# Optimization experiments

Measured on AMD Instinct MI355X. Metric: run time of the kernel, lower is better.

The kernel has to match this reference:

```python
import jax, jax.numpy as jnp
import numpy as np
from jax import lax

V, E, C_OUT, K, NTAGS = 32000, 256, 256, 3, 32
B, T = 64, 2048


def setup_inputs() -> dict:
    key = jax.random.key(0)
    ks = jax.random.split(key, 12)
    inputs = jax.random.randint(ks[0], (B, T), 0, V)
    emb_table = jax.random.normal(ks[1], (V, E), jnp.float32) * 0.02
    emb_table = emb_table.at[1].set(0.0)  # padding_idx=1
    conv1_w = jax.random.normal(ks[2], (C_OUT, E, K), jnp.float32) * 0.02
    conv1_b = jax.random.normal(ks[3], (C_OUT,), jnp.float32) * 0.02
    conv2_w = jax.random.normal(ks[4], (C_OUT, C_OUT, K), jnp.float32) * 0.02
    conv2_b = jax.random.normal(ks[5], (C_OUT,), jnp.float32) * 0.02
    fc_w = jax.random.normal(ks[6], (NTAGS, E), jnp.float32) * 0.02
    fc_b = jax.random.normal(ks[7], (NTAGS,), jnp.float32) * 0.02
    trans = jax.random.normal(ks[8], (NTAGS, NTAGS), jnp.float32) * 0.1
    start_t = jax.random.normal(ks[9], (NTAGS,), jnp.float32) * 0.1
    end_t = jax.random.normal(ks[10], (NTAGS,), jnp.float32) * 0.1
    return {"inputs": inputs, "emb_table": emb_table,
            "conv1_w": conv1_w, "conv1_b": conv1_b,
            "conv2_w": conv2_w, "conv2_b": conv2_b,
            "fc_w": fc_w, "fc_b": fc_b,
            "trans": trans, "start_t": start_t, "end_t": end_t}


def _conv1d(x, w, b):
    # x: [B, C_in, T], w: [C_out, C_in, K], padding=1
    y = lax.conv_general_dilated(x, w, window_strides=(1,), padding=[(1, 1)],
                                 dimension_numbers=("NCH", "OIH", "NCH"))
    return y + b[None, :, None]


def _crf_log_partition(emissions, trans, start_t, end_t):
    # emissions: [B, T, NTAGS] -> logZ per sequence [B]
    em_t = jnp.swapaxes(emissions, 0, 1)  # [T, B, NTAGS]
    alpha0 = start_t[None, :] + em_t[0]   # [B, NTAGS]

    def step(alpha, emit):
        # alpha: [B, C]; broadcast prev-tag x next-tag: [B, C, C]
        scores = alpha[:, :, None] + trans[None, :, :] + emit[:, None, :]
        new_alpha = jax.scipy.special.logsumexp(scores, axis=1)
        return new_alpha, None

    alpha, _ = lax.scan(step, alpha0, em_t[1:])
    return jax.scipy.special.logsumexp(alpha + end_t[None, :], axis=-1)


def reference(inputs, emb_table, conv1_w, conv1_b, conv2_w, conv2_b,
              fc_w, fc_b, trans, start_t, end_t):
    emb = emb_table[inputs]                    # [B, T, E]
    x = jnp.swapaxes(emb, 1, 2)                # [B, E, T]
    x = _conv1d(x, conv1_w, conv1_b)           # [B, C, T]
    x = _conv1d(x, conv2_w, conv2_b)           # [B, C, T]
    h = jnp.swapaxes(x, 1, 2)                  # [B, T, E]  (dropout = identity in eval)
    logits = jnp.einsum("bte,ce->btc", h, fc_w) + fc_b  # [B, T, NTAGS]
    return _crf_log_partition(logits, trans, start_t, end_t)  # [B]
```

## Files before the change

### kernel.cpp

```cpp
#include <hip/hip_runtime.h>
#include <hip/hip_bf16.h>

typedef float f32x4 __attribute__((ext_vector_type(4)));
typedef __bf16 bf16x8 __attribute__((ext_vector_type(8)));
typedef __bf16 bf16x4 __attribute__((ext_vector_type(4)));

__global__ __launch_bounds__(256) void transpose_w(const float* __restrict__ w1,
                                                   const float* __restrict__ w2,
                                                   float* __restrict__ w1t,
                                                   float* __restrict__ w2t) {
  int tid = blockIdx.x * 256 + threadIdx.x;
  if (tid < 196608) {
    float v = w1[tid];
    int k1 = tid % 3;
    int r = tid / 3;
    int e = r & 255;
    int cp = r >> 8;
    w1t[(k1 * 256 + e) * 256 + cp] = v;
  } else {
    int t2 = tid - 196608;
    float v = w2[t2];
    int k2 = t2 % 3;
    int r = t2 / 3;
    int cp = r & 255;
    int c = r >> 8;
    w2t[(k2 * 256 + cp) * 256 + c] = v;
  }
}

__global__ __launch_bounds__(256) void prep_g(const float* __restrict__ fcw,
                                              const float* __restrict__ w2t,
                                              float* __restrict__ G) {
  int tid = blockIdx.x * 256 + threadIdx.x;
  int cp = tid & 255;
  int rest = tid >> 8;
  int n = rest & 31;
  int k2 = rest >> 5;
  const float* wr = w2t + (k2 * 256 + cp) * 256;
  const float* fr = fcw + n * 256;
  float acc = 0.f;
  #pragma unroll 8
  for (int c = 0; c < 256; c += 4) {
    f32x4 a = *(const f32x4*)(fr + c);
    f32x4 bb = *(const f32x4*)(wr + c);
    acc = fmaf(a[0], bb[0], acc); acc = fmaf(a[1], bb[1], acc);
    acc = fmaf(a[2], bb[2], acc); acc = fmaf(a[3], bb[3], acc);
  }
  G[(k2 * 32 + n) * 256 + cp] = acc;
}

__global__ __launch_bounds__(256) void prep_wf(const float* __restrict__ G,
                                               const float* __restrict__ w1t,
                                               const float* __restrict__ b1,
                                               const float* __restrict__ b2,
                                               const float* __restrict__ fcw,
                                               const float* __restrict__ fcb,
                                               __bf16* __restrict__ wfb,
                                               float* __restrict__ C0,
                                               float* __restrict__ CT,
                                               float* __restrict__ bias_tot,
                                               float* __restrict__ c0v,
                                               float* __restrict__ cTv) {
  int tid = blockIdx.x * 256 + threadIdx.x;
  if (tid < 40960) {
    int n = tid & 31;
    int r = tid >> 5;
    int kk = r % 5;
    int e = r / 5;
    float acc = 0.f;
    #pragma unroll
    for (int k2 = 0; k2 < 3; ++k2) {
      int k1 = kk - k2;
      if (k1 < 0 || k1 > 2) continue;
      const float* g = G + (k2 * 32 + n) * 256;
      const float* wr = w1t + (k1 * 256 + e) * 256;
      #pragma unroll 8
      for (int cp = 0; cp < 256; cp += 4) {
        f32x4 a = *(const f32x4*)(g + cp);
        f32x4 bb = *(const f32x4*)(wr + cp);
        acc = fmaf(a[0], bb[0], acc); acc = fmaf(a[1], bb[1], acc);
        acc = fmaf(a[2], bb[2], acc); acc = fmaf(a[3], bb[3], acc);
      }
    }
    int j = kk * 32 + n;
    int jt = j >> 4, jl = j & 15;
    int et = e >> 5, el = e & 31;
    int lane = jl | ((el >> 3) << 4);
    int rr = el & 7;
    wfb[((jt * 8 + et) * 64 + lane) * 8 + rr] = (__bf16)acc;
  } else if (tid < 57344) {
    int t2 = tid - 40960;
    int which = (t2 >= 8192);
    if (which) t2 -= 8192;
    int n = t2 & 31;
    int e = t2 >> 5;
    const float* g = G + ((which ? 2 : 0) * 32 + n) * 256;
    int k1 = which ? 0 : 2;
    const float* wr = w1t + (k1 * 256 + e) * 256;
    float acc = 0.f;
    #pragma unroll 8
    for (int cp = 0; cp < 256; cp += 4) {
      f32x4 a = *(const f32x4*)(g + cp);
      f32x4 bb = *(const f32x4*)(wr + cp);
      acc = fmaf(a[0], bb[0], acc); acc = fmaf(a[1], bb[1], acc);
      acc = fmaf(a[2], bb[2], acc); acc = fmaf(a[3], bb[3], acc);
    }
    (which ? CT : C0)[n * 256 + e] = acc;
  } else if (tid < 57376) {
    int n = tid - 57344;
    float bt = fcb[n];
    for (int c = 0; c < 256; ++c) bt = fmaf(fcw[n * 256 + c], b2[c], bt);
    float s0 = 0.f, s1 = 0.f, s2 = 0.f;
    const float* g0 = G + (0 * 32 + n) * 256;
    const float* g1 = G + (1 * 32 + n) * 256;
    const float* g2 = G + (2 * 32 + n) * 256;
    for (int cp = 0; cp < 256; ++cp) {
      s0 = fmaf(g0[cp], b1[cp], s0);
      s1 = fmaf(g1[cp], b1[cp], s1);
      s2 = fmaf(g2[cp], b1[cp], s2);
    }
    bias_tot[n] = bt + s0 + s1 + s2;
    c0v[n] = s0;
    cTv[n] = s2;
  }
}

__global__ __launch_bounds__(256) void ptab_corr(const float* __restrict__ emb,
                                                 const __bf16* __restrict__ wfb,
                                                 __bf16* __restrict__ P,
                                                 const int* __restrict__ idx,
                                                 const float* __restrict__ C0,
                                                 const float* __restrict__ CT,
                                                 const float* __restrict__ c0v,
                                                 const float* __restrict__ cTv,
                                                 float* __restrict__ corr) {
  __shared__ float red[256];
  if (blockIdx.x < 500) {
    int lane = threadIdx.x & 63;
    int mt = blockIdx.x * 4 + (threadIdx.x >> 6);
    int ln = lane & 15;
    int q = lane >> 4;
    int m = mt * 16 + ln;
    f32x4 acc[10];
    #pragma unroll
    for (int jt = 0; jt < 10; ++jt) acc[jt] = (f32x4){0.f, 0.f, 0.f, 0.f};
    const float* arow = emb + m * 256 + q * 8;
    #pragma unroll
    for (int et = 0; et < 8; ++et) {
      f32x4 a0 = *(const f32x4*)(arow + et * 32);
      f32x4 a1 = *(const f32x4*)(arow + et * 32 + 4);
      bf16x8 af;
      af[0] = (__bf16)a0[0]; af[1] = (__bf16)a0[1];
      af[2] = (__bf16)a0[2]; af[3] = (__bf16)a0[3];
      af[4] = (__bf16)a1[0]; af[5] = (__bf16)a1[1];
      af[6] = (__bf16)a1[2]; af[7] = (__bf16)a1[3];
      #pragma unroll
      for (int jt = 0; jt < 10; ++jt) {
        bf16x8 bfr = *(const bf16x8*)(wfb + ((jt * 8 + et) * 64 + lane) * 8);
        acc[jt] = __builtin_amdgcn_mfma_f32_16x16x32_bf16(af, bfr, acc[jt], 0, 0, 0);
      }
    }
    #pragma unroll
    for (int jt = 0; jt < 10; ++jt) {
      __bf16* pp = P + (mt * 16 + q * 4) * 160 + jt * 16 + ln;
      pp[0]   = (__bf16)acc[jt][0];
      pp[160] = (__bf16)acc[jt][1];
      pp[320] = (__bf16)acc[jt][2];
      pp[480] = (__bf16)acc[jt][3];
    }
  } else {
    int bid = blockIdx.x - 500;
    int b = bid >> 1;
    int which = bid & 1;
    int n = threadIdx.x & 31;
    int part = threadIdx.x >> 5;
    int v = idx[b * 2048 + (which ? 2047 : 0)];
    const float* C = which ? CT : C0;
    const float* er = emb + v * 256 + part * 32;
    const float* cr = C + n * 256 + part * 32;
    float s = 0.f;
    #pragma unroll
    for (int e = 0; e < 32; ++e) s = fmaf(cr[e], er[e], s);
    red[threadIdx.x] = s;
    __syncthreads();
    if (part == 0) {
      float tot = (which ? cTv : c0v)[n];
      #pragma unroll
      for (int p = 0; p < 8; ++p) tot += red[p * 32 + n];
      corr[(which * 64 + b) * 32 + n] = tot;
    }
  }
}

#define LROW 164
__global__ __launch_bounds__(256) void logits_k(const int* __restrict__ idx,
                                                const __bf16* __restrict__ P,
                                                const float* __restrict__ bias_tot,
                                                const float* __restrict__ corr,
                                                __bf16* __restrict__ L) {
  __shared__ __bf16 sp[132 * LROW];
  int b = blockIdx.x >> 4;
  int tb = blockIdx.x & 15;
  int t0 = tb * 128;
  const int* ib = idx + b * 2048;
  for (int ch = threadIdx.x; ch < 2640; ch += 256) {
    int r = ch / 20;
    int part = ch - r * 20;
    int t = t0 - 2 + r;
    uint4 val = {0u, 0u, 0u, 0u};
    if (t >= 0 && t < 2048) {
      int v = ib[t];
      val = *(const uint4*)((const char*)(P + v * 160) + part * 16);
    }
    *(uint4*)((char*)(sp + r * LROW) + part * 16) = val;
  }
  __syncthreads();
  int q = threadIdx.x & 7;
  int ts = threadIdx.x >> 3;
  f32x4 bias = *(const f32x4*)(bias_tot + q * 4);
  f32x4 corr0 = *(const f32x4*)(corr + b * 32 + q * 4);
  f32x4 corrT = *(const f32x4*)(corr + (64 + b) * 32 + q * 4);
  #pragma unroll
  for (int i = 0; i < 4; ++i) {
    int tl = ts + 32 * i;
    int t = t0 + tl;
    f32x4 acc = bias;
    #pragma unroll
    for (int k = 0; k < 5; ++k) {
      bf16x4 pv = *(const bf16x4*)(sp + (tl + k) * LROW + k * 32 + q * 4);
      acc[0] += (float)pv[0]; acc[1] += (float)pv[1];
      acc[2] += (float)pv[2]; acc[3] += (float)pv[3];
    }
    if (t == 0)    acc -= corr0;
    if (t == 2047) acc -= corrT;
    bf16x4 r;
    r[0] = (__bf16)(__expf(acc[0]) * 0.03125f);
    r[1] = (__bf16)(__expf(acc[1]) * 0.03125f);
    r[2] = (__bf16)(__expf(acc[2]) * 0.03125f);
    r[3] = (__bf16)(__expf(acc[3]) * 0.03125f);
    *(bf16x4*)(L + (b * 2048 + t) * 32 + q * 4) = r;
  }
}

__global__ __launch_bounds__(256) void crf_stage1(const __bf16* __restrict__ Lexp,
                                                  const float* __restrict__ trans,
                                                  __bf16* __restrict__ PcB) {
  __shared__ __bf16 sl[4][32 * 40];
  int lane = threadIdx.x & 63;
  int w = threadIdx.x >> 6;
  int chain = blockIdx.x * 4 + w;
  int c = chain >> 6;
  int b = chain & 63;
  int ln = lane & 15;
  int q = lane >> 4;
  float tA0[8], tA1[8];
  #pragma unroll
  for (int e = 0; e < 8; ++e) {
    tA0[e] = __expf(trans[(q * 8 + e) * 32 + ln]);
    tA1[e] = __expf(trans[(q * 8 + e) * 32 + 16 + ln]);
  }
  bf16x8 bf0, bf1;
  #pragma unroll
  for (int e = 0; e < 8; ++e) {
    int k = q * 8 + e;
    bf0[e] = (k == ln) ? (__bf16)1.0f : (__bf16)0.0f;
    bf1[e] = (k == 16 + ln) ? (__bf16)1.0f : (__bf16)0.0f;
  }
  int tstart = c * 32 + 1;
  int total = (c == 63) ? 31 : 32;
  const __bf16* Le = Lexp + (b * 2048 + tstart) * 32;
  __bf16* myS = &sl[w][0];

  auto step = [&](float sc0, float sc1) {
    bf16x8 a0, a1;
    #pragma unroll
    for (int e = 0; e < 8; ++e) {
      a0[e] = (__bf16)(sc0 * tA0[e]);
      a1[e] = (__bf16)(sc1 * tA1[e]);
    }
    f32x4 z = {0.f, 0.f, 0.f, 0.f};
    f32x4 c00 = __builtin_amdgcn_mfma_f32_16x16x32_bf16(a0, bf0, z, 0, 0, 0);
    f32x4 c01 = __builtin_amdgcn_mfma_f32_16x16x32_bf16(a0, bf1, z, 0, 0, 0);
    f32x4 c10 = __builtin_amdgcn_mfma_f32_16x16x32_bf16(a1, bf0, z, 0, 0, 0);
    f32x4 c11 = __builtin_amdgcn_mfma_f32_16x16x32_bf16(a1, bf1, z, 0, 0, 0);
    bf16x4 w00, w01, w10, w11;
    #pragma unroll
    for (int r = 0; r < 4; ++r) {
      w00[r] = (__bf16)c00[r]; w01[r] = (__bf16)c01[r];
      w10[r] = (__bf16)c10[r]; w11[r] = (__bf16)c11[r];
    }
    *(bf16x4*)(myS + (ln) * 40      + q * 4)      = w00;
    *(bf16x4*)(myS + (16 + ln) * 40 + q * 4)      = w01;
    *(bf16x4*)(myS + (ln) * 40      + 16 + q * 4) = w10;
    *(bf16x4*)(myS + (16 + ln) * 40 + 16 + q * 4) = w11;
    bf0 = *(const bf16x8*)(myS + (ln) * 40 + q * 8);
    bf1 = *(const bf16x8*)(myS + (16 + ln) * 40 + q * 8);
  };

  float s0[8], s1[8];
  #pragma unroll
  for (int i = 0; i < 8; ++i) {
    s0[i] = (float)Le[i * 32 + ln];
    s1[i] = (float)Le[i * 32 + 16 + ln];
  }
  int nbatch = total >> 3;
  int rem = total & 7;
  for (int bt = 0; bt < nbatch; ++bt) {
    float n0[8], n1[8];
    bool more = (bt + 1 < nbatch) || (rem != 0 && bt + 1 == nbatch);
    if (more) {
      int bs = (bt + 1) * 8;
      #pragma unroll
      for (int i = 0; i < 8; ++i) {
        int k = bs + i; if (k >= total) k = total - 1;
        n0[i] = (float)Le[k * 32 + ln];
        n1[i] = (float)Le[k * 32 + 16 + ln];
      }
    }
    #pragma unroll
    for (int s = 0; s < 8; ++s) step(s0[s], s1[s]);
    #pragma unroll
    for (int i = 0; i < 8; ++i) { s0[i] = n0[i]; s1[i] = n1[i]; }
  }
  if (rem) {
    #pragma unroll
    for (int s = 0; s < 7; ++s) step(s0[s], s1[s]);
  }
  bf16x8 o0, o1;
  #pragma unroll
  for (int e = 0; e < 8; ++e) {
    o0[e] = myS[(q * 8 + e) * 40 + ln];
    o1[e] = myS[(q * 8 + e) * 40 + 16 + ln];
  }
  __bf16* dst = PcB + ((b * 64 + c) * 64 + lane) * 16;
  *(bf16x8*)(dst)     = o0;
  *(bf16x8*)(dst + 8) = o1;
}

__global__ __launch_bounds__(512) void crf_tail(const __bf16* __restrict__ Lexp,
                                                const __bf16* __restrict__ PcB,
                                                const float* __restrict__ start_t,
                                                const float* __restrict__ end_t,
                                                float* __restrict__ out) {
  __shared__ float sg[8][1024];
  __shared__ __bf16 sl[8][32 * 40];
  int b = blockIdx.x;
  int tid = threadIdx.x;
  int lane = tid & 63;
  int g = tid >> 6;
  int ln = lane & 15;
  int q = lane >> 4;
  const __bf16* base = PcB + ((b * 64 + g * 8) * 64) * 16;
  bf16x8 a0 = *(const bf16x8*)(base + lane * 16);
  bf16x8 a1 = *(const bf16x8*)(base + lane * 16 + 8);
  bf16x8 bf0, bf1;
  #pragma unroll
  for (int e = 0; e < 8; ++e) {
    int k = q * 8 + e;
    bf0[e] = (k == ln) ? (__bf16)1.0f : (__bf16)0.0f;
    bf1[e] = (k == 16 + ln) ? (__bf16)1.0f : (__bf16)0.0f;
  }
  __bf16* myS = &sl[g][0];
  f32x4 c00, c01, c10, c11;
  for (int j = 0; j < 8; ++j) {
    bf16x8 na0, na1;
    if (j < 7) {
      const __bf16* nb = base + (j + 1) * 1024 + lane * 16;
      na0 = *(const bf16x8*)(nb);
      na1 = *(const bf16x8*)(nb + 8);
    }
    f32x4 z = {0.f, 0.f, 0.f, 0.f};
    c00 = __builtin_amdgcn_mfma_f32_16x16x32_bf16(a0, bf0, z, 0, 0, 0);
    c01 = __builtin_amdgcn_mfma_f32_16x16x32_bf16(a0, bf1, z, 0, 0, 0);
    c10 = __builtin_amdgcn_mfma_f32_16x16x32_bf16(a1, bf0, z, 0, 0, 0);
    c11 = __builtin_amdgcn_mfma_f32_16x16x32_bf16(a1, bf1, z, 0, 0, 0);
    if (j < 7) {
      bf16x4 w00, w01, w10, w11;
      #pragma unroll
      for (int r = 0; r < 4; ++r) {
        w00[r] = (__bf16)c00[r]; w01[r] = (__bf16)c01[r];
        w10[r] = (__bf16)c10[r]; w11[r] = (__bf16)c11[r];
      }
      *(bf16x4*)(myS + (ln) * 40      + q * 4)      = w00;
      *(bf16x4*)(myS + (16 + ln) * 40 + q * 4)      = w01;
      *(bf16x4*)(myS + (ln) * 40      + 16 + q * 4) = w10;
      *(bf16x4*)(myS + (16 + ln) * 40 + 16 + q * 4) = w11;
      bf0 = *(const bf16x8*)(myS + (ln) * 40 + q * 8);
      bf1 = *(const bf16x8*)(myS + (16 + ln) * 40 + q * 8);
      a0 = na0; a1 = na1;
    }
  }
  #pragma unroll
  for (int r = 0; r < 4; ++r) {
    sg[g][(ln) * 32      + q * 4 + r]      = c00[r];
    sg[g][(16 + ln) * 32 + q * 4 + r]      = c01[r];
    sg[g][(ln) * 32      + 16 + q * 4 + r] = c10[r];
    sg[g][(16 + ln) * 32 + 16 + q * 4 + r] = c11[r];
  }
  int j2 = tid & 31;
  float u = __expf(start_t[j2]) * (float)Lexp[b * 2048 * 32 + j2] * 32.f;
  __syncthreads();
  float logacc = 0.f;
  #pragma unroll
  for (int gg = 0; gg < 8; ++gg) {
    const float* M = &sg[gg][0];
    float nu0 = 0.f, nu1 = 0.f, nu2 = 0.f, nu3 = 0.f;
    #pragma unroll
    for (int k = 0; k < 32; k += 4) {
      nu0 = fmaf(__shfl(u, k,     32), M[(k)     * 32 + j2], nu0);
      nu1 = fmaf(__shfl(u, k + 1, 32), M[(k + 1) * 32 + j2], nu1);
      nu2 = fmaf(__shfl(u, k + 2, 32), M[(k + 2) * 32 + j2], nu2);
      nu3 = fmaf(__shfl(u, k + 3, 32), M[(k + 3) * 32 + j2], nu3);
    }
    float nu = (nu0 + nu1) + (nu2 + nu3);
    float ssum = nu;
    #pragma unroll
    for (int o = 1; o < 32; o <<= 1) ssum += __shfl_xor(ssum, o, 32);
    u = nu * __builtin_amdgcn_rcpf(ssum);
    logacc += __logf(ssum);
  }
  float term = u * __expf(end_t[j2]);
  #pragma unroll
  for (int o = 1; o < 32; o <<= 1) term += __shfl_xor(term, o, 32);
  if (tid == 0)
    out[b] = logacc + logf(term) + (float)(2047.0 * 5.0 * 0.69314718055994530942);
}

extern "C" void kernel_launch(void* const* d_in, const int* in_sizes, int n_in,
                              void* d_out, int out_size, void* d_ws, size_t ws_size,
                              hipStream_t stream) {
  const int*   idx  = (const int*)d_in[0];
  const float* emb  = (const float*)d_in[1];
  const float* w1   = (const float*)d_in[2];
  const float* b1   = (const float*)d_in[3];
  const float* w2   = (const float*)d_in[4];
  const float* b2   = (const float*)d_in[5];
  const float* fcw  = (const float*)d_in[6];
  const float* fcb  = (const float*)d_in[7];
  const float* trn  = (const float*)d_in[8];
  const float* st   = (const float*)d_in[9];
  const float* en   = (const float*)d_in[10];

  char* ws = (char*)d_ws;
  __bf16* P     = (__bf16*)(ws + 0);
  __bf16* L     = (__bf16*)(ws + 10240000);
  __bf16* PcB   = (__bf16*)(ws + 18628608);
  float*  w1t   = (float*)(ws + 27017216);
  float*  w2t   = (float*)(ws + 27803648);
  __bf16* WfB   = (__bf16*)(ws + 43794432);
  float*  G     = (float*)(ws + 43876352);
  float*  C0    = (float*)(ws + 43974656);
  float*  CT    = (float*)(ws + 44007424);
  float*  bias  = (float*)(ws + 44040192);
  float*  c0v   = (float*)(ws + 44040320);
  float*  cTv   = (float*)(ws + 44040448);
  float*  corr  = (float*)(ws + 44040576);

  transpose_w<<<1536, 256, 0, stream>>>(w1, w2, w1t, w2t);
  prep_g     <<<96,   256, 0, stream>>>(fcw, w2t, G);
  prep_wf    <<<225,  256, 0, stream>>>(G, w1t, b1, b2, fcw, fcb, WfB, C0, CT, bias, c0v, cTv);
  ptab_corr  <<<628,  256, 0, stream>>>(emb, WfB, P, idx, C0, CT, c0v, cTv, corr);
  logits_k   <<<1024, 256, 0, stream>>>(idx, P, bias, corr, L);
  crf_stage1 <<<1024, 256, 0, stream>>>(L, trn, PcB);
  crf_tail   <<<64,   512, 0, stream>>>(L, PcB, st, en, (float*)d_out);
}
```

Measured before the change: 199.7 us.

## Fuse logits computation into CRF stage-1 chunk kernel via shared memory

```diff
diff --git a/kernel.cpp b/kernel.cpp
--- a/kernel.cpp
+++ b/kernel.cpp
@@ -192,86 +192,81 @@
   }
 }
 
-#define LROW 164
-__global__ __launch_bounds__(256) void logits_k(const int* __restrict__ idx,
-                                                const __bf16* __restrict__ P,
-                                                const float* __restrict__ bias_tot,
-                                                const float* __restrict__ corr,
-                                                __bf16* __restrict__ L) {
-  __shared__ __bf16 sp[132 * LROW];
+__global__ __launch_bounds__(256) void logits_crf1(const int* __restrict__ idx,
+                                                   const __bf16* __restrict__ P,
+                                                   const float* __restrict__ bias_tot,
+                                                   const float* __restrict__ corr,
+                                                   const float* __restrict__ trans,
+                                                   __bf16* __restrict__ PcB,
+                                                   float* __restrict__ Lt0) {
+  __shared__ __bf16 sLe[129 * 32];
+  __shared__ __bf16 sl[4][32 * 40];
   int b = blockIdx.x >> 4;
   int tb = blockIdx.x & 15;
   int t0 = tb * 128;
-  const int* ib = idx + b * 2048;
-  for (int ch = threadIdx.x; ch < 2640; ch += 256) {
-    int r = ch / 20;
-    int part = ch - r * 20;
-    int t = t0 - 2 + r;
-    uint4 val = {0u, 0u, 0u, 0u};
-    if (t >= 0 && t < 2048) {
-      int v = ib[t];
-      val = *(const uint4*)((const char*)(P + v * 160) + part * 16);
-    }
-    *(uint4*)((char*)(sp + r * LROW) + part * 16) = val;
+  int tid = threadIdx.x;
+  int lane = tid & 63;
+  int w = tid >> 6;
+  int ln = lane & 15;
+  int q4 = lane >> 4;
+  float tA0[8], tA1[8];
+  #pragma unroll
+  for (int e = 0; e < 8; ++e) {
+    tA0[e] = __expf(trans[(q4 * 8 + e) * 32 + ln]);
+    tA1[e] = __expf(trans[(q4 * 8 + e) * 32 + 16 + ln]);
+  }
+  {
+    int q = tid & 7;
+    int ts0 = tid >> 3;
+    const int* ib = idx + b * 2048;
+    f32x4 bias = *(const f32x4*)(bias_tot + q * 4);
+    f32x4 corr0 = *(const f32x4*)(corr + b * 32 + q * 4);
+    f32x4 corrT = *(const f32x4*)(corr + (64 + b) * 32 + q * 4);
+    int nts = (ts0 == 0 && tb < 15) ? 5 : 4;
+    for (int i = 0; i < nts; ++i) {
+      int ts = ts0 + 32 * i;
+      int t = t0 + ts;
+      f32x4 acc = bias;
+      #pragma unroll
+      for (int k = 0; k < 5; ++k) {
+        int tt = t + k - 2;
+        if (tt >= 0 && tt < 2048) {
+          int v = ib[tt];
+          bf16x4 pv = *(const bf16x4*)(P + v * 160 + k * 32 + q * 4);
+          acc[0] += (float)pv[0]; acc[1] += (float)pv[1];
+          acc[2] += (float)pv[2]; acc[3] += (float)pv[3];
+        }
+      }
+      if (t == 0)    acc -= corr0;
+      if (t == 2047) acc -= corrT;
+      float e0 = __expf(acc[0]) * 0.03125f;
+      float e1 = __expf(acc[1]) * 0.03125f;
+      float e2 = __expf(acc[2]) * 0.03125f;
+      float e3 = __expf(acc[3]) * 0.03125f;
+      bf16x4 r;
+      r[0] = (__bf16)e0; r[1] = (__bf16)e1; r[2] = (__bf16)e2; r[3] = (__bf16)e3;
+      *(bf16x4*)(sLe + ts * 32 + q * 4) = r;
+      if (t == 0) {
+        float* d = Lt0 + b * 32 + q * 4;
+        d[0] = e0; d[1] = e1; d[2] = e2; d[3] = e3;
+      }
+    }
   }
   __syncthreads();
-  int q = threadIdx.x & 7;
-  int ts = threadIdx.x >> 3;
-  f32x4 bias = *(const f32x4*)(bias_tot + q * 4);
-  f32x4 corr0 = *(const f32x4*)(corr + b * 32 + q * 4);
-  f32x4 corrT = *(const f32x4*)(corr + (64 + b) * 32 + q * 4);
-  #pragma unroll
-  for (int i = 0; i < 4; ++i) {
-    int tl = ts + 32 * i;
-    int t = t0 + tl;
-    f32x4 acc = bias;
-    #pragma unroll
-    for (int k = 0; k < 5; ++k) {
-      bf16x4 pv = *(const bf16x4*)(sp + (tl + k) * LROW + k * 32 + q * 4);
-      acc[0] += (float)pv[0]; acc[1] += (float)pv[1];
-      acc[2] += (float)pv[2]; acc[3] += (float)pv[3];
-    }
-    if (t == 0)    acc -= corr0;
-    if (t == 2047) acc -= corrT;
-    bf16x4 r;
-    r[0] = (__bf16)(__expf(acc[0]) * 0.03125f);
-    r[1] = (__bf16)(__expf(acc[1]) * 0.03125f);
-    r[2] = (__bf16)(__expf(acc[2]) * 0.03125f);
-    r[3] = (__bf16)(__expf(acc[3]) * 0.03125f);
-    *(bf16x4*)(L + (b * 2048 + t) * 32 + q * 4) = r;
-  }
-}
-
-__global__ __launch_bounds__(256) void crf_stage1(const __bf16* __restrict__ Lexp,
-                                                  const float* __restrict__ trans,
-                                                  __bf16* __restrict__ PcB) {
-  __shared__ __bf16 sl[4][32 * 40];
-  int lane = threadIdx.x & 63;
-  int w = threadIdx.x >> 6;
-  int chain = blockIdx.x * 4 + w;
-  int c = chain >> 6;
-  int b = chain & 63;
-  int ln = lane & 15;
-  int q = lane >> 4;
-  float tA0[8], tA1[8];
+  int c = tb * 4 + w;
+  int nsteps = (c == 63) ? 31 : 32;
+  bf16x8 bf0, bf1;
   #pragma unroll
   for (int e = 0; e < 8; ++e) {
-    tA0[e] = __expf(trans[(q * 8 + e) * 32 + ln]);
-    tA1[e] = __expf(trans[(q * 8 + e) * 32 + 16 + ln]);
-  }
-  bf16x8 bf0, bf1;
-  #pragma unroll
-  for (int e = 0; e < 8; ++e) {
-    int k = q * 8 + e;
+    int k = q4 * 8 + e;
     bf0[e] = (k == ln) ? (__bf16)1.0f : (__bf16)0.0f;
     bf1[e] = (k == 16 + ln) ? (__bf16)1.0f : (__bf16)0.0f;
   }
-  int tstart = c * 32 + 1;
-  int total = (c == 63) ? 31 : 32;
-  const __bf16* Le = Lexp + (b * 2048 + tstart) * 32;
   __bf16* myS = &sl[w][0];
-
-  auto step = [&](float sc0, float sc1) {
+  for (int s = 0; s < nsteps; ++s) {
+    int lts = w * 32 + 1 + s;
+    float sc0 = (float)sLe[lts * 32 + ln];
+    float sc1 = (float)sLe[lts * 32 + 16 + ln];
     bf16x8 a0, a1;
     #pragma unroll
     for (int e = 0; e < 8; ++e) {
@@ -289,55 +284,25 @@
       w00[r] = (__bf16)c00[r]; w01[r] = (__bf16)c01[r];
       w10[r] = (__bf16)c10[r]; w11[r] = (__bf16)c11[r];
     }
-    *(bf16x4*)(myS + (ln) * 40      + q * 4)      = w00;
-    *(bf16x4*)(myS + (16 + ln) * 40 + q * 4)      = w01;
-    *(bf16x4*)(myS + (ln) * 40      + 16 + q * 4) = w10;
-    *(bf16x4*)(myS + (16 + ln) * 40 + 16 + q * 4) = w11;
-    bf0 = *(const bf16x8*)(myS + (ln) * 40 + q * 8);
-    bf1 = *(const bf16x8*)(myS + (16 + ln) * 40 + q * 8);
-  };
-
-  float s0[8], s1[8];
-  #pragma unroll
-  for (int i = 0; i < 8; ++i) {
-    s0[i] = (float)Le[i * 32 + ln];
-    s1[i] = (float)Le[i * 32 + 16 + ln];
-  }
-  int nbatch = total >> 3;
-  int rem = total & 7;
-  for (int bt = 0; bt < nbatch; ++bt) {
-    float n0[8], n1[8];
-    bool more = (bt + 1 < nbatch) || (rem != 0 && bt + 1 == nbatch);
-    if (more) {
-      int bs = (bt + 1) * 8;
-      #pragma unroll
-      for (int i = 0; i < 8; ++i) {
-        int k = bs + i; if (k >= total) k = total - 1;
-        n0[i] = (float)Le[k * 32 + ln];
-        n1[i] = (float)Le[k * 32 + 16 + ln];
-      }
-    }
-    #pragma unroll
-    for (int s = 0; s < 8; ++s) step(s0[s], s1[s]);
-    #pragma unroll
-    for (int i = 0; i < 8; ++i) { s0[i] = n0[i]; s1[i] = n1[i]; }
-  }
-  if (rem) {
-    #pragma unroll
-    for (int s = 0; s < 7; ++s) step(s0[s], s1[s]);
+    *(bf16x4*)(myS + (ln) * 40      + q4 * 4)      = w00;
+    *(bf16x4*)(myS + (16 + ln) * 40 + q4 * 4)      = w01;
+    *(bf16x4*)(myS + (ln) * 40      + 16 + q4 * 4) = w10;
+    *(bf16x4*)(myS + (16 + ln) * 40 + 16 + q4 * 4) = w11;
+    bf0 = *(const bf16x8*)(myS + (ln) * 40 + q4 * 8);
+    bf1 = *(const bf16x8*)(myS + (16 + ln) * 40 + q4 * 8);
   }
   bf16x8 o0, o1;
   #pragma unroll
   for (int e = 0; e < 8; ++e) {
-    o0[e] = myS[(q * 8 + e) * 40 + ln];
-    o1[e] = myS[(q * 8 + e) * 40 + 16 + ln];
+    o0[e] = myS[(q4 * 8 + e) * 40 + ln];
+    o1[e] = myS[(q4 * 8 + e) * 40 + 16 + ln];
   }
   __bf16* dst = PcB + ((b * 64 + c) * 64 + lane) * 16;
   *(bf16x8*)(dst)     = o0;
   *(bf16x8*)(dst + 8) = o1;
 }
 
-__global__ __launch_bounds__(512) void crf_tail(const __bf16* __restrict__ Lexp,
+__global__ __launch_bounds__(512) void crf_tail(const float* __restrict__ Lt0,
                                                 const __bf16* __restrict__ PcB,
                                                 const float* __restrict__ start_t,
                                                 const float* __restrict__ end_t,
@@ -398,7 +363,7 @@
     sg[g][(16 + ln) * 32 + 16 + q * 4 + r] = c11[r];
   }
   int j2 = tid & 31;
-  float u = __expf(start_t[j2]) * (float)Lexp[b * 2048 * 32 + j2] * 32.f;
+  float u = __expf(start_t[j2]) * Lt0[b * 32 + j2] * 32.f;
   __syncthreads();
   float logacc = 0.f;
   #pragma unroll
@@ -443,24 +408,23 @@
 
   char* ws = (char*)d_ws;
   __bf16* P     = (__bf16*)(ws + 0);
-  __bf16* L     = (__bf16*)(ws + 10240000);
-  __bf16* PcB   = (__bf16*)(ws + 18628608);
-  float*  w1t   = (float*)(ws + 27017216);
-  float*  w2t   = (float*)(ws + 27803648);
-  __bf16* WfB   = (__bf16*)(ws + 43794432);
-  float*  G     = (float*)(ws + 43876352);
-  float*  C0    = (float*)(ws + 43974656);
-  float*  CT    = (float*)(ws + 44007424);
-  float*  bias  = (float*)(ws + 44040192);
-  float*  c0v   = (float*)(ws + 44040320);
-  float*  cTv   = (float*)(ws + 44040448);
-  float*  corr  = (float*)(ws + 44040576);
+  __bf16* PcB   = (__bf16*)(ws + 10240000);
+  float*  w1t   = (float*)(ws + 18628608);
+  float*  w2t   = (float*)(ws + 19415040);
+  __bf16* WfB   = (__bf16*)(ws + 20201472);
+  float*  G     = (float*)(ws + 20283392);
+  float*  C0    = (float*)(ws + 20381696);
+  float*  CT    = (float*)(ws + 20414464);
+  float*  bias  = (float*)(ws + 20447232);
+  float*  c0v   = (float*)(ws + 20447360);
+  float*  cTv   = (float*)(ws + 20447488);
+  float*  corr  = (float*)(ws + 20447616);
+  float*  Lt0   = (float*)(ws + 20464000);
 
   transpose_w<<<1536, 256, 0, stream>>>(w1, w2, w1t, w2t);
   prep_g     <<<96,   256, 0, stream>>>(fcw, w2t, G);
   prep_wf    <<<225,  256, 0, stream>>>(G, w1t, b1, b2, fcw, fcb, WfB, C0, CT, bias, c0v, cTv);
   ptab_corr  <<<628,  256, 0, stream>>>(emb, WfB, P, idx, C0, CT, c0v, cTv, corr);
-  logits_k   <<<1024, 256, 0, stream>>>(idx, P, bias, corr, L);
-  crf_stage1 <<<1024, 256, 0, stream>>>(L, trn, PcB);
-  crf_tail   <<<64,   512, 0, stream>>>(L, PcB, st, en, (float*)d_out);
-}
+  logits_crf1<<<1024, 256, 0, stream>>>(idx, P, bias, corr, trn, PcB, Lt0);
+  crf_tail   <<<64,   512, 0, stream>>>(Lt0, PcB, st, en, (float*)d_out);
+}
```

New measurement: 193.1 us. 3.3% less time.
